# Kernel optimization log

Hardware: AMD Instinct MI355X
Metric: run time of the kernel (lower is better)

## Reference

```python
import jax, jax.numpy as jnp
import numpy as np

NDIMS = 3  # 3D affine: trf has NDIMS*(NDIMS+1) = 12 params per sample
BATCH = 4194304


def setup_inputs() -> dict:
    key = jax.random.key(0)
    # scale by 0.1 so eye + shift stays comfortably invertible
    trf = jax.random.normal(key, (BATCH, NDIMS * (NDIMS + 1)), dtype=jnp.float32) * 0.1
    return {"trf": trf}


def reference(trf):
    """Batched InvertAffine: shift -> identity-form homogeneous matrix,
    invert, -> shift form. Fully vectorized (no map_fn)."""
    B = trf.shape[0]
    n = NDIMS
    eye = jnp.eye(n + 1, dtype=trf.dtype)
    mat = trf.reshape(B, n, n + 1)                      # (B, n, n+1)
    bottom = jnp.zeros((B, 1, n + 1), dtype=trf.dtype)  # homogeneous last row
    full = jnp.concatenate([mat, bottom], axis=1) + eye  # (B, n+1, n+1), identity added
    inv = jnp.linalg.inv(full)                           # batched small inverse
    shift = inv - eye                                    # back to shift representation
    return shift[:, :n, :].reshape(B, n * (n + 1))
```

## Files before the change

kernel.cpp:

```cpp
#include <hip/hip_runtime.h>


#define PAD 13
#define TILE 256
#define WSAMP 64

__device__ __forceinline__ void invert12(const float* __restrict__ p,
                                         float* __restrict__ q) {
  const float a00 = p[0] + 1.0f, a01 = p[1],        a02 = p[2],         t0 = p[3];
  const float a10 = p[4],        a11 = p[5] + 1.0f, a12 = p[6],         t1 = p[7];
  const float a20 = p[8],        a21 = p[9],        a22 = p[10] + 1.0f, t2 = p[11];

  const float c00 = a11 * a22 - a12 * a21;
  const float c01 = a12 * a20 - a10 * a22;
  const float c02 = a10 * a21 - a11 * a20;

  const float det  = a00 * c00 + a01 * c01 + a02 * c02;
  const float rdet = 1.0f / det;

  const float i00 = c00 * rdet;
  const float i01 = (a02 * a21 - a01 * a22) * rdet;
  const float i02 = (a01 * a12 - a02 * a11) * rdet;
  const float i10 = c01 * rdet;
  const float i11 = (a00 * a22 - a02 * a20) * rdet;
  const float i12 = (a02 * a10 - a00 * a12) * rdet;
  const float i20 = c02 * rdet;
  const float i21 = (a01 * a20 - a00 * a21) * rdet;
  const float i22 = (a00 * a11 - a01 * a10) * rdet;

  q[0] = i00 - 1.0f; q[1]  = i01;        q[2]  = i02;
  q[3] = -(i00 * t0 + i01 * t1 + i02 * t2);
  q[4] = i10;        q[5]  = i11 - 1.0f; q[6]  = i12;
  q[7] = -(i10 * t0 + i11 * t1 + i12 * t2);
  q[8] = i20;        q[9]  = i21;        q[10] = i22 - 1.0f;
  q[11] = -(i20 * t0 + i21 * t1 + i22 * t2);
}

__global__ __launch_bounds__(256) void invert_affine_kernel(
    const float4* __restrict__ in, float4* __restrict__ out, int nTiles, int B) {
  __shared__ float lds[(TILE / WSAMP) * WSAMP * PAD];
  const int t = threadIdx.x;
  const int w = t >> 6;
  const int l = t & 63;
  float* __restrict__ wlds = &lds[w * (WSAMP * PAD)];

  int off[3];
#pragma unroll
  for (int k = 0; k < 3; ++k) {
    const int j = k * WSAMP + l;
    const int s = j / 3, r = j - 3 * s;
    off[k] = PAD * s + 4 * r;
  }

  for (int tile = blockIdx.x; tile < nTiles; tile += gridDim.x) {
    const long long base = (long long)tile * (TILE * 3) + w * (WSAMP * 3);

#pragma unroll
    for (int k = 0; k < 3; ++k) {
      const float4 v = in[base + k * WSAMP + l];
      float* p = &wlds[off[k]];
      p[0] = v.x; p[1] = v.y; p[2] = v.z; p[3] = v.w;
    }
    __builtin_amdgcn_wave_barrier();

    float res[12];
    invert12(&wlds[PAD * l], res);
    __builtin_amdgcn_wave_barrier();

#pragma unroll
    for (int c = 0; c < 12; ++c) wlds[PAD * l + c] = res[c];
    __builtin_amdgcn_wave_barrier();

#pragma unroll
    for (int k = 0; k < 3; ++k) {
      const float* p = &wlds[off[k]];
      out[base + k * WSAMP + l] = make_float4(p[0], p[1], p[2], p[3]);
    }
    __builtin_amdgcn_wave_barrier();
  }

  const int tailStart = nTiles * TILE;
  for (int i = tailStart + blockIdx.x * (int)blockDim.x + t; i < B;
       i += gridDim.x * blockDim.x) {
    float buf[12], res[12];
    const float4 r0 = in[3 * (long long)i + 0];
    const float4 r1 = in[3 * (long long)i + 1];
    const float4 r2 = in[3 * (long long)i + 2];
    buf[0] = r0.x; buf[1] = r0.y; buf[2]  = r0.z; buf[3]  = r0.w;
    buf[4] = r1.x; buf[5] = r1.y; buf[6]  = r1.z; buf[7]  = r1.w;
    buf[8] = r2.x; buf[9] = r2.y; buf[10] = r2.z; buf[11] = r2.w;
    invert12(buf, res);
    out[3 * (long long)i + 0] = make_float4(res[0], res[1], res[2], res[3]);
    out[3 * (long long)i + 1] = make_float4(res[4], res[5], res[6], res[7]);
    out[3 * (long long)i + 2] = make_float4(res[8], res[9], res[10], res[11]);
  }
}

extern "C" void kernel_launch(void* const* d_in, const int* in_sizes, int n_in,
                              void* d_out, int out_size, void* d_ws, size_t ws_size,
                              hipStream_t stream) {
  (void)n_in; (void)d_ws; (void)ws_size; (void)out_size;
  const float4* in4 = (const float4*)d_in[0];
  float4* out4 = (float4*)d_out;
  const int B = in_sizes[0] / 12;
  const int nTiles = B / TILE;

  int blocks = nTiles > 0 ? nTiles : 1;
  if (blocks > 2048) blocks = 2048;

  invert_affine_kernel<<<blocks, 256, 0, stream>>>(in4, out4, nTiles, B);
}
```

Baseline: 79.37 us.

## Prefetch next tile in registers with contiguous per-block ranges and nontemporal access

Each block now processes a contiguous range of tiles instead of a grid-strided set, and software-pipelines the loop by issuing the next tile's global loads before processing the current tile. Global loads and stores use nontemporal builtins to avoid cache pollution on this streaming kernel. One wave barrier between compute and the LDS write-back is dropped. The added prefetch raises register use, and contiguous chunks change the DRAM access pattern across blocks.

```diff
diff --git a/kernel.cpp b/kernel.cpp
--- a/kernel.cpp
+++ b/kernel.cpp
@@ -1,5 +1,7 @@
 #include <hip/hip_runtime.h>
 
+
+typedef float f4 __attribute__((ext_vector_type(4)));
 
 #define PAD 13
 #define TILE 256
@@ -37,7 +39,8 @@
 }
 
 __global__ __launch_bounds__(256) void invert_affine_kernel(
-    const float4* __restrict__ in, float4* __restrict__ out, int nTiles, int B) {
+    const f4* __restrict__ in, f4* __restrict__ out,
+    int nTiles, int B, int per) {
   __shared__ float lds[(TILE / WSAMP) * WSAMP * PAD];
   const int t = threadIdx.x;
   const int w = t >> 6;
@@ -52,47 +55,72 @@
     off[k] = PAD * s + 4 * r;
   }
 
-  for (int tile = blockIdx.x; tile < nTiles; tile += gridDim.x) {
-    const long long base = (long long)tile * (TILE * 3) + w * (WSAMP * 3);
+  const int tileBeg = blockIdx.x * per;
+  const int tileEnd = (tileBeg + per < nTiles) ? tileBeg + per : nTiles;
+
+  if (tileBeg < tileEnd) {
+    long long base = (long long)tileBeg * (TILE * 3) + w * (WSAMP * 3);
+
+    f4 cur0 = __builtin_nontemporal_load(&in[base + 0 * WSAMP + l]);
+    f4 cur1 = __builtin_nontemporal_load(&in[base + 1 * WSAMP + l]);
+    f4 cur2 = __builtin_nontemporal_load(&in[base + 2 * WSAMP + l]);
+
+    for (int tile = tileBeg; tile < tileEnd; ++tile) {
+      f4 nxt0, nxt1, nxt2;
+      const bool more = (tile + 1) < tileEnd;
+      if (more) {
+        const long long nb = base + (TILE * 3);
+        nxt0 = __builtin_nontemporal_load(&in[nb + 0 * WSAMP + l]);
+        nxt1 = __builtin_nontemporal_load(&in[nb + 1 * WSAMP + l]);
+        nxt2 = __builtin_nontemporal_load(&in[nb + 2 * WSAMP + l]);
+      }
+
+      {
+        float* p0 = &wlds[off[0]];
+        p0[0] = cur0.x; p0[1] = cur0.y; p0[2] = cur0.z; p0[3] = cur0.w;
+        float* p1 = &wlds[off[1]];
+        p1[0] = cur1.x; p1[1] = cur1.y; p1[2] = cur1.z; p1[3] = cur1.w;
+        float* p2 = &wlds[off[2]];
+        p2[0] = cur2.x; p2[1] = cur2.y; p2[2] = cur2.z; p2[3] = cur2.w;
+      }
+      __builtin_amdgcn_wave_barrier();
+
+      float res[12];
+      invert12(&wlds[PAD * l], res);
+#pragma unroll
+      for (int c = 0; c < 12; ++c) wlds[PAD * l + c] = res[c];
+      __builtin_amdgcn_wave_barrier();
 
 #pragma unroll
-    for (int k = 0; k < 3; ++k) {
-      const float4 v = in[base + k * WSAMP + l];
-      float* p = &wlds[off[k]];
-      p[0] = v.x; p[1] = v.y; p[2] = v.z; p[3] = v.w;
+      for (int k = 0; k < 3; ++k) {
+        const float* p = &wlds[off[k]];
+        f4 v; v.x = p[0]; v.y = p[1]; v.z = p[2]; v.w = p[3];
+        __builtin_nontemporal_store(v, &out[base + k * WSAMP + l]);
+      }
+      __builtin_amdgcn_wave_barrier();
+
+      cur0 = nxt0; cur1 = nxt1; cur2 = nxt2;
+      base += TILE * 3;
     }
-    __builtin_amdgcn_wave_barrier();
-
-    float res[12];
-    invert12(&wlds[PAD * l], res);
-    __builtin_amdgcn_wave_barrier();
-
-#pragma unroll
-    for (int c = 0; c < 12; ++c) wlds[PAD * l + c] = res[c];
-    __builtin_amdgcn_wave_barrier();
-
-#pragma unroll
-    for (int k = 0; k < 3; ++k) {
-      const float* p = &wlds[off[k]];
-      out[base + k * WSAMP + l] = make_float4(p[0], p[1], p[2], p[3]);
-    }
-    __builtin_amdgcn_wave_barrier();
   }
 
   const int tailStart = nTiles * TILE;
   for (int i = tailStart + blockIdx.x * (int)blockDim.x + t; i < B;
        i += gridDim.x * blockDim.x) {
     float buf[12], res[12];
-    const float4 r0 = in[3 * (long long)i + 0];
-    const float4 r1 = in[3 * (long long)i + 1];
-    const float4 r2 = in[3 * (long long)i + 2];
+    const f4 r0 = in[3 * (long long)i + 0];
+    const f4 r1 = in[3 * (long long)i + 1];
+    const f4 r2 = in[3 * (long long)i + 2];
     buf[0] = r0.x; buf[1] = r0.y; buf[2]  = r0.z; buf[3]  = r0.w;
     buf[4] = r1.x; buf[5] = r1.y; buf[6]  = r1.z; buf[7]  = r1.w;
     buf[8] = r2.x; buf[9] = r2.y; buf[10] = r2.z; buf[11] = r2.w;
     invert12(buf, res);
-    out[3 * (long long)i + 0] = make_float4(res[0], res[1], res[2], res[3]);
-    out[3 * (long long)i + 1] = make_float4(res[4], res[5], res[6], res[7]);
-    out[3 * (long long)i + 2] = make_float4(res[8], res[9], res[10], res[11]);
+    f4 o0; o0.x = res[0]; o0.y = res[1];  o0.z = res[2];  o0.w = res[3];
+    f4 o1; o1.x = res[4]; o1.y = res[5];  o1.z = res[6];  o1.w = res[7];
+    f4 o2; o2.x = res[8]; o2.y = res[9];  o2.z = res[10]; o2.w = res[11];
+    out[3 * (long long)i + 0] = o0;
+    out[3 * (long long)i + 1] = o1;
+    out[3 * (long long)i + 2] = o2;
   }
 }
 
@@ -100,13 +128,14 @@
                               void* d_out, int out_size, void* d_ws, size_t ws_size,
                               hipStream_t stream) {
   (void)n_in; (void)d_ws; (void)ws_size; (void)out_size;
-  const float4* in4 = (const float4*)d_in[0];
-  float4* out4 = (float4*)d_out;
+  const f4* in4 = (const f4*)d_in[0];
+  f4* out4 = (f4*)d_out;
   const int B = in_sizes[0] / 12;
   const int nTiles = B / TILE;
 
   int blocks = nTiles > 0 ? nTiles : 1;
   if (blocks > 2048) blocks = 2048;
+  const int per = (nTiles + blocks - 1) / blocks;
 
-  invert_affine_kernel<<<blocks, 256, 0, stream>>>(in4, out4, nTiles, B);
+  invert_affine_kernel<<<blocks, 256, 0, stream>>>(in4, out4, nTiles, B, per);
 }
```

Result: faster. 77.37 us (-2.5%).
